# Performance work log

Hardware: AMD Instinct MI355X
Metric: run time of the kernel (lower is better)

## Reference

```python
import jax, jax.numpy as jnp
import numpy as np

COMMITMENT_COST = 0.25


def setup_inputs() -> dict:
    key = jax.random.key(0)
    k1, k2 = jax.random.split(key)
    inputs = jax.random.normal(k1, (32, 64, 64, 64), dtype=jnp.float32)  # BCHW, C=embedding_dim
    codebook = jax.random.normal(k2, (1024, 64), dtype=jnp.float32)      # [n_embeddings, embedding_dim]
    return {"inputs": inputs, "codebook": codebook}


def reference(inputs, codebook):
    B, C, H, W = inputs.shape
    K, D = codebook.shape  # D == C
    x = jnp.transpose(inputs, (0, 2, 3, 1))          # BHWC
    flat = x.reshape(-1, D)                          # [N, D]
    # squared-euclidean distances [N, K]
    distances = (jnp.sum(flat * flat, axis=1, keepdims=True)
                 + jnp.sum(codebook * codebook, axis=1)
                 - 2.0 * flat @ codebook.T)
    logits = -distances
    idx = jnp.argmax(logits, axis=-1)                # [N]
    oh = jax.nn.one_hot(idx, K, dtype=flat.dtype)    # [N, K]
    # straight-through one-hot
    oh_st = oh + logits - jax.lax.stop_gradient(logits)
    oh_encodings = jnp.transpose(oh_st.reshape(B, H * W, K), (0, 2, 1))  # b d n
    # quantized computed under no_grad in torch -> full stop_gradient
    quantized = jax.lax.stop_gradient(oh_st @ codebook).reshape(x.shape)  # BHWC
    e_latent_loss = jnp.mean((quantized - x) ** 2)
    loss = COMMITMENT_COST * e_latent_loss
    q_st = x + jax.lax.stop_gradient(quantized - x)  # straight-through output
    avg_probs = jnp.mean(oh_st, axis=0)              # [K]
    perplexity = jnp.exp(-jnp.sum(avg_probs * jnp.log(avg_probs + 1e-10)))
    return (loss, jnp.transpose(q_st, (0, 3, 1, 2)), perplexity, oh_encodings)
```

## Files before the change

### kernel.cpp

```cpp
#include <hip/hip_runtime.h>
#include <math.h>

typedef _Float16 half8 __attribute__((ext_vector_type(8)));
typedef float f32x4 __attribute__((ext_vector_type(4)));

#define NBLK_TOT 1536
#define Q_OFF    1
#define PERP_OFF 8388609
#define OH_OFF   8388610
#define LOSS_N   8388608.0f
#define OH_F4_BASE 8388612
#define OH_NF4     33554431

#define CB2_OFF_B 16384
#define IDX_OFF_W 69632

__global__ __launch_bounds__(256) void k0_prep(const float* __restrict__ cb,
                                               float* __restrict__ cnorm,
                                               int* __restrict__ hist,
                                               char* __restrict__ cb2) {
  int k = blockIdx.x * 256 + threadIdx.x;
  hist[k] = 0;
  const float* row = cb + (size_t)k * 64;
  const float4* r4 = (const float4*)row;
  float s = 0.f;
#pragma unroll
  for (int i = 0; i < 16; ++i) {
    float4 v = r4[i];
    s += v.x * v.x + v.y * v.y + v.z * v.z + v.w * v.w;
  }
  cnorm[k] = s;

  int tile = k >> 4, c = k & 15;
  char* base = cb2 + tile * 4096;
#pragma unroll
  for (int d16 = 0; d16 < 8; ++d16) {
    half8 hh, ll;
#pragma unroll
    for (int i = 0; i < 8; ++i) {
      float v = row[d16 * 8 + i];
      _Float16 h = (_Float16)v;
      hh[i] = h;
      ll[i] = (_Float16)(v - (float)h);
    }
    int off = (d16 >> 2) * 1024 + c * 64 + (d16 & 3) * 16;
    *(half8*)(base + off) = hh;
    *(half8*)(base + 2048 + off) = ll;
  }
}

__global__ __launch_bounds__(256, 4) void k1_main(
    const float* __restrict__ in, const float* __restrict__ cb,
    const char* __restrict__ cb2, const float* __restrict__ cnorm,
    int* __restrict__ hist, float* __restrict__ partial,
    int* __restrict__ idx, float* __restrict__ out) {
  __shared__ int bestk_s[128];
  __shared__ float red[256];

  const int tid = threadIdx.x;
  const int bid = blockIdx.x;
  const int r3 = bid % 3;

  if (r3 == 2) {
    const int fi = bid / 3;
    float4* base = (float4*)(out + OH_F4_BASE);
    const float4 z4 = make_float4(0.f, 0.f, 0.f, 0.f);
    const size_t b0 = (size_t)fi * 65536 + tid;
    if (fi < 511) {
#pragma unroll 8
      for (int i = 0; i < 256; ++i) base[b0 + (size_t)i * 256] = z4;
    } else {
#pragma unroll 8
      for (int i = 0; i < 256; ++i) {
        size_t i4 = b0 + (size_t)i * 256;
        if (i4 < OH_NF4) base[i4] = z4;
      }
      if (tid == 0) {
        out[OH_OFF] = 0.f; out[OH_OFF + 1] = 0.f;
        out[OH_F4_BASE + 4 * (size_t)OH_NF4] = 0.f;
        out[OH_F4_BASE + 4 * (size_t)OH_NF4 + 1] = 0.f;
      }
    }
    return;
  }

  const int ci = (bid / 3) * 2 + r3;
  const int b = ci >> 5;
  const int hw0 = (ci & 31) << 7;
  const int w = tid >> 6, l = tid & 63, q = l & 15, g = l >> 4;

  half8 ah[2][2], al[2][2];
  {
    const float* xb = in + ((size_t)b << 18);
#pragma unroll
    for (int a = 0; a < 2; ++a) {
      const int hw = hw0 + w * 32 + a * 16 + q;
#pragma unroll
      for (int ks = 0; ks < 2; ++ks) {
#pragma unroll
        for (int i = 0; i < 8; ++i) {
          float v = xb[((size_t)(ks * 32 + g * 8 + i) << 12) + hw];
          _Float16 h = (_Float16)v;
          ah[a][ks][i] = h;
          al[a][ks][i] = (_Float16)(v - (float)h);
        }
      }
    }
  }

  float bd0[4], bd1[4];
  int bk0[4], bk1[4];
#pragma unroll
  for (int j = 0; j < 4; ++j) { bd0[j] = bd1[j] = 3.4e38f; bk0[j] = bk1[j] = 0; }

  const int boff = q * 64 + g * 16;

  for (int tb = 0; tb < 64; ++tb) {
    const char* tbase = cb2 + tb * 4096 + boff;
    half8 bh0 = *(const half8*)(tbase);
    half8 bh1 = *(const half8*)(tbase + 1024);
    half8 bl0 = *(const half8*)(tbase + 2048);
    half8 bl1 = *(const half8*)(tbase + 3072);
    const int code = tb * 16 + q;
    const float cn = cnorm[code];
    const f32x4 z = {0.f, 0.f, 0.f, 0.f};
    f32x4 s = __builtin_amdgcn_mfma_f32_16x16x32_f16(ah[0][0], bh0, z, 0, 0, 0);
    s = __builtin_amdgcn_mfma_f32_16x16x32_f16(al[0][0], bh0, s, 0, 0, 0);
    s = __builtin_amdgcn_mfma_f32_16x16x32_f16(ah[0][0], bl0, s, 0, 0, 0);
    f32x4 t = __builtin_amdgcn_mfma_f32_16x16x32_f16(ah[0][1], bh1, z, 0, 0, 0);
    t = __builtin_amdgcn_mfma_f32_16x16x32_f16(al[0][1], bh1, t, 0, 0, 0);
    t = __builtin_amdgcn_mfma_f32_16x16x32_f16(ah[0][1], bl1, t, 0, 0, 0);
    s = s + t;
#pragma unroll
    for (int j = 0; j < 4; ++j) {
      float d = fmaf(-2.f, s[j], cn);
      if (d < bd0[j]) { bd0[j] = d; bk0[j] = code; }
    }
    f32x4 u = __builtin_amdgcn_mfma_f32_16x16x32_f16(ah[1][0], bh0, z, 0, 0, 0);
    u = __builtin_amdgcn_mfma_f32_16x16x32_f16(al[1][0], bh0, u, 0, 0, 0);
    u = __builtin_amdgcn_mfma_f32_16x16x32_f16(ah[1][0], bl0, u, 0, 0, 0);
    f32x4 v = __builtin_amdgcn_mfma_f32_16x16x32_f16(ah[1][1], bh1, z, 0, 0, 0);
    v = __builtin_amdgcn_mfma_f32_16x16x32_f16(al[1][1], bh1, v, 0, 0, 0);
    v = __builtin_amdgcn_mfma_f32_16x16x32_f16(ah[1][1], bl1, v, 0, 0, 0);
    u = u + v;
#pragma unroll
    for (int j = 0; j < 4; ++j) {
      float d = fmaf(-2.f, u[j], cn);
      if (d < bd1[j]) { bd1[j] = d; bk1[j] = code; }
    }
  }

#pragma unroll
  for (int m = 1; m < 16; m <<= 1) {
#pragma unroll
    for (int j = 0; j < 4; ++j) {
      float od = __shfl_xor(bd0[j], m, 64);
      int ok = __shfl_xor(bk0[j], m, 64);
      if (od < bd0[j] || (od == bd0[j] && ok < bk0[j])) { bd0[j] = od; bk0[j] = ok; }
      od = __shfl_xor(bd1[j], m, 64);
      ok = __shfl_xor(bk1[j], m, 64);
      if (od < bd1[j] || (od == bd1[j] && ok < bk1[j])) { bd1[j] = od; bk1[j] = ok; }
    }
  }
  if (q == 0) {
#pragma unroll
    for (int j = 0; j < 4; ++j) {
      bestk_s[w * 32 + g * 4 + j] = bk0[j];
      bestk_s[w * 32 + 16 + g * 4 + j] = bk1[j];
    }
  }
  __syncthreads();

  const int p = tid & 127, hf = tid >> 7;
  const int kq = bestk_s[p];
  if (hf == 0) {
    idx[ci * 128 + p] = kq;
    atomicAdd(&hist[kq], 1);
  }
  float lsum = 0.f;
  {
    const float* xb = in + ((size_t)b << 18) + hw0 + p;
    float* yb = out + Q_OFF + ((size_t)b << 18) + hw0 + p;
    const float* qrow = cb + (size_t)kq * 64;
#pragma unroll
    for (int c = 0; c < 32; ++c) {
      const int cc = hf * 32 + c;
      float x = xb[(size_t)cc << 12];
      float f = qrow[cc] - x;
      lsum += f * f;
      yb[(size_t)cc << 12] = x + f;
    }
  }
  red[tid] = lsum;
  __syncthreads();
#pragma unroll
  for (int sft = 128; sft > 0; sft >>= 1) {
    if (tid < sft) red[tid] += red[tid + sft];
    __syncthreads();
  }
  if (tid == 0) partial[ci] = red[0];
}

__global__ __launch_bounds__(1024) void k2_finalize(const int* __restrict__ hist,
                                                    const float* __restrict__ partial,
                                                    float* __restrict__ out) {
  __shared__ float red[1024];
  int tid = threadIdx.x;

  red[tid] = partial[tid];
  __syncthreads();
  for (int s = 512; s > 0; s >>= 1) {
    if (tid < s) red[tid] += red[tid + s];
    __syncthreads();
  }
  if (tid == 0) out[0] = 0.25f * (red[0] / LOSS_N);
  __syncthreads();

  float pr = (float)hist[tid] * (1.0f / 131072.0f);
  red[tid] = pr * logf(pr + 1e-10f);
  __syncthreads();
  for (int s = 512; s > 0; s >>= 1) {
    if (tid < s) red[tid] += red[tid + s];
    __syncthreads();
  }
  if (tid == 0) out[PERP_OFF] = expf(-red[0]);
}

__global__ __launch_bounds__(256) void k3_scatter(const int* __restrict__ idx,
                                                  float* __restrict__ out) {
  int n = blockIdx.x * 256 + threadIdx.x;
  int k = idx[n];
  int b = n >> 12;
  int pos = n & 4095;
  out[OH_OFF + ((((size_t)b << 10) + (size_t)k) << 12) + pos] = 1.0f;
}

extern "C" void kernel_launch(void* const* d_in, const int* in_sizes, int n_in,
                              void* d_out, int out_size, void* d_ws, size_t ws_size,
                              hipStream_t stream) {
  const float* in = (const float*)d_in[0];
  const float* cb = (const float*)d_in[1];
  float* out = (float*)d_out;

  float* cnorm   = (float*)d_ws;
  int*   hist    = (int*)d_ws + 1024;
  float* partial = (float*)d_ws + 2048;
  char*  cb2b    = (char*)d_ws + CB2_OFF_B;
  int*   idx     = (int*)d_ws + IDX_OFF_W;

  k0_prep<<<4, 256, 0, stream>>>(cb, cnorm, hist, cb2b);
  k1_main<<<NBLK_TOT, 256, 0, stream>>>(in, cb, cb2b, cnorm, hist, partial, idx, out);
  k2_finalize<<<1, 1024, 0, stream>>>(hist, partial, out);
  k3_scatter<<<512, 256, 0, stream>>>(idx, out);
}
```

Before: 223.0 us.

## Split one-hot zero-fill into separate kernel and scatter ones from compute kernel

The zero-fill of the 512MB one-hot output moves out of the interleaved main kernel into a dedicated fill kernel launched first. The compute kernel then writes the one-hot 1.0 entries directly, which removes the index buffer and the separate scatter kernel. The cost is that fill and compute no longer overlap inside one launch, so the compute stage waits for the bandwidth-bound fill to finish.

```diff
diff --git a/kernel.cpp b/kernel.cpp
--- a/kernel.cpp
+++ b/kernel.cpp
@@ -4,7 +4,6 @@
 typedef _Float16 half8 __attribute__((ext_vector_type(8)));
 typedef float f32x4 __attribute__((ext_vector_type(4)));
 
-#define NBLK_TOT 1536
 #define Q_OFF    1
 #define PERP_OFF 8388609
 #define OH_OFF   8388610
@@ -13,7 +12,6 @@
 #define OH_NF4     33554431
 
 #define CB2_OFF_B 16384
-#define IDX_OFF_W 69632
 
 __global__ __launch_bounds__(256) void k0_prep(const float* __restrict__ cb,
                                                float* __restrict__ cnorm,
@@ -49,44 +47,40 @@
   }
 }
 
-__global__ __launch_bounds__(256, 4) void k1_main(
+__global__ __launch_bounds__(256) void k_fill(float* __restrict__ out) {
+  const int tid = threadIdx.x;
+  float4* base = (float4*)(out + OH_F4_BASE);
+  const float4 z4 = make_float4(0.f, 0.f, 0.f, 0.f);
+  const size_t b0 = (size_t)blockIdx.x * 16384 + tid;
+  if (blockIdx.x < 2047) {
+#pragma unroll 8
+    for (int i = 0; i < 64; ++i) base[b0 + (size_t)i * 256] = z4;
+  } else {
+#pragma unroll 8
+    for (int i = 0; i < 64; ++i) {
+      size_t i4 = b0 + (size_t)i * 256;
+      if (i4 < OH_NF4) base[i4] = z4;
+    }
+    if (tid == 0) {
+      out[OH_OFF] = 0.f; out[OH_OFF + 1] = 0.f;
+      out[OH_F4_BASE + 4 * (size_t)OH_NF4] = 0.f;
+      out[OH_F4_BASE + 4 * (size_t)OH_NF4 + 1] = 0.f;
+    }
+  }
+}
+
+__global__ __launch_bounds__(256, 4) void k_compute(
     const float* __restrict__ in, const float* __restrict__ cb,
     const char* __restrict__ cb2, const float* __restrict__ cnorm,
     int* __restrict__ hist, float* __restrict__ partial,
-    int* __restrict__ idx, float* __restrict__ out) {
+    float* __restrict__ out) {
   __shared__ int bestk_s[128];
   __shared__ float red[256];
 
   const int tid = threadIdx.x;
   const int bid = blockIdx.x;
-  const int r3 = bid % 3;
-
-  if (r3 == 2) {
-    const int fi = bid / 3;
-    float4* base = (float4*)(out + OH_F4_BASE);
-    const float4 z4 = make_float4(0.f, 0.f, 0.f, 0.f);
-    const size_t b0 = (size_t)fi * 65536 + tid;
-    if (fi < 511) {
-#pragma unroll 8
-      for (int i = 0; i < 256; ++i) base[b0 + (size_t)i * 256] = z4;
-    } else {
-#pragma unroll 8
-      for (int i = 0; i < 256; ++i) {
-        size_t i4 = b0 + (size_t)i * 256;
-        if (i4 < OH_NF4) base[i4] = z4;
-      }
-      if (tid == 0) {
-        out[OH_OFF] = 0.f; out[OH_OFF + 1] = 0.f;
-        out[OH_F4_BASE + 4 * (size_t)OH_NF4] = 0.f;
-        out[OH_F4_BASE + 4 * (size_t)OH_NF4 + 1] = 0.f;
-      }
-    }
-    return;
-  }
-
-  const int ci = (bid / 3) * 2 + r3;
-  const int b = ci >> 5;
-  const int hw0 = (ci & 31) << 7;
+  const int b = bid >> 5;
+  const int hw0 = (bid & 31) << 7;
   const int w = tid >> 6, l = tid & 63, q = l & 15, g = l >> 4;
 
   half8 ah[2][2], al[2][2];
@@ -174,7 +168,7 @@
   const int p = tid & 127, hf = tid >> 7;
   const int kq = bestk_s[p];
   if (hf == 0) {
-    idx[ci * 128 + p] = kq;
+    out[OH_OFF + ((size_t)b << 22) + ((size_t)kq << 12) + hw0 + p] = 1.0f;
     atomicAdd(&hist[kq], 1);
   }
   float lsum = 0.f;
@@ -198,7 +192,7 @@
     if (tid < sft) red[tid] += red[tid + sft];
     __syncthreads();
   }
-  if (tid == 0) partial[ci] = red[0];
+  if (tid == 0) partial[bid] = red[0];
 }
 
 __global__ __launch_bounds__(1024) void k2_finalize(const int* __restrict__ hist,
@@ -224,15 +218,6 @@
     __syncthreads();
   }
   if (tid == 0) out[PERP_OFF] = expf(-red[0]);
-}
-
-__global__ __launch_bounds__(256) void k3_scatter(const int* __restrict__ idx,
-                                                  float* __restrict__ out) {
-  int n = blockIdx.x * 256 + threadIdx.x;
-  int k = idx[n];
-  int b = n >> 12;
-  int pos = n & 4095;
-  out[OH_OFF + ((((size_t)b << 10) + (size_t)k) << 12) + pos] = 1.0f;
 }
 
 extern "C" void kernel_launch(void* const* d_in, const int* in_sizes, int n_in,
@@ -246,10 +231,9 @@
   int*   hist    = (int*)d_ws + 1024;
   float* partial = (float*)d_ws + 2048;
   char*  cb2b    = (char*)d_ws + CB2_OFF_B;
-  int*   idx     = (int*)d_ws + IDX_OFF_W;
 
   k0_prep<<<4, 256, 0, stream>>>(cb, cnorm, hist, cb2b);
-  k1_main<<<NBLK_TOT, 256, 0, stream>>>(in, cb, cb2b, cnorm, hist, partial, idx, out);
+  k_fill<<<2048, 256, 0, stream>>>(out);
+  k_compute<<<1024, 256, 0, stream>>>(in, cb, cb2b, cnorm, hist, partial, out);
   k2_finalize<<<1, 1024, 0, stream>>>(hist, partial, out);
-  k3_scatter<<<512, 256, 0, stream>>>(idx, out);
-}
+}
```

Measured after the change: 279.5 us. 1.25x slower.
